# Optimization experiments

Measured on AMD Instinct MI355X. Metric: run time of the kernel, lower is better.

The kernel has to match this reference:

```python
import jax, jax.numpy as jnp
import numpy as np

B, L, D, H = 32, 1024, 1024, 1024

def setup_inputs() -> dict:
    key = jax.random.key(0)
    k1, k2, k3 = jax.random.split(key, 3)
    query = jax.random.normal(k1, (B, L, D), dtype=jnp.float32)
    keys = jax.random.normal(k2, (B, L, D), dtype=jnp.float32)
    # xavier_normal for Linear(D, H): std = sqrt(2/(D+H))
    W = jax.random.normal(k3, (H, D), dtype=jnp.float32) * np.sqrt(2.0 / (D + H)).astype(np.float32)
    b = jnp.zeros((H,), dtype=jnp.float32)
    return {"query": query, "keys": keys, "W": W, "b": b}

def reference(query, keys, W, b):
    # L2-normalize along feature dim (matches torch .norm(dim=-1, keepdim=True))
    qn = query / jnp.linalg.norm(query, axis=-1, keepdims=True)
    kn = keys / jnp.linalg.norm(keys, axis=-1, keepdims=True)
    # scores[b,i,j] = <kn[b,i], qn[b,j]>  ->  [B, Lk, Lq]
    scores = jnp.einsum('bid,bjd->bij', kn, qn)
    attn = jax.nn.softmax(scores, axis=-1)
    # bmm(attn, keys) then sum over batch -> [L, D]
    out = jnp.einsum('bij,bjd->id', attn, keys)
    x = jax.nn.relu(out @ W.T + b)
    return (x, attn)
```

## Files before the change

### kernel.cpp

```cpp
#include <hip/hip_runtime.h>
#include <hip/hip_bf16.h>

#define NBATCH 32
#define Ls 1024
#define Ds 1024
#define Hs 1024

typedef float f32x4 __attribute__((ext_vector_type(4)));
typedef __bf16 v8bf __attribute__((ext_vector_type(8)));
typedef unsigned short u16x8 __attribute__((ext_vector_type(8)));
typedef unsigned short u16x4 __attribute__((ext_vector_type(4)));
typedef __hip_bfloat16 bf16;

__device__ __forceinline__ float bfbits2f(unsigned short h) {
  unsigned u = ((unsigned)h) << 16;
  return __builtin_bit_cast(float, u);
}
__device__ __forceinline__ unsigned short f2b(float x) {
  return __builtin_bit_cast(unsigned short, __float2bfloat16(x));
}
__device__ __forceinline__ u16x8 pack8(const float4& a, const float4& b, float s) {
  u16x8 r;
  r[0] = f2b(a.x * s); r[1] = f2b(a.y * s); r[2] = f2b(a.z * s); r[3] = f2b(a.w * s);
  r[4] = f2b(b.x * s); r[5] = f2b(b.y * s); r[6] = f2b(b.z * s); r[7] = f2b(b.w * s);
  return r;
}

__global__ __launch_bounds__(256) void k_convq(const float* __restrict__ q,
                                               bf16* __restrict__ qn) {
  const int w0 = ((int)blockIdx.x * 256 + (int)threadIdx.x) >> 6;
  const int lane = threadIdx.x & 63;
  #pragma unroll
  for (int it = 0; it < 2; ++it) {
    const size_t r0 = ((size_t)(it * 8192 + w0)) * 2;
    const float4* q0 = reinterpret_cast<const float4*>(q + r0 * Ds);
    float4 qv[2][4];
    #pragma unroll
    for (int rr = 0; rr < 2; ++rr)
      #pragma unroll
      for (int h = 0; h < 2; ++h) {
        qv[rr][h * 2 + 0] = q0[rr * 256 + h * 128 + lane * 2 + 0];
        qv[rr][h * 2 + 1] = q0[rr * 256 + h * 128 + lane * 2 + 1];
      }
    float sq0 = 0.f, sq1 = 0.f;
    #pragma unroll
    for (int p = 0; p < 4; ++p) {
      sq0 += qv[0][p].x*qv[0][p].x + qv[0][p].y*qv[0][p].y + qv[0][p].z*qv[0][p].z + qv[0][p].w*qv[0][p].w;
      sq1 += qv[1][p].x*qv[1][p].x + qv[1][p].y*qv[1][p].y + qv[1][p].z*qv[1][p].z + qv[1][p].w*qv[1][p].w;
    }
    #pragma unroll
    for (int o = 1; o < 64; o <<= 1) { sq0 += __shfl_xor(sq0, o); sq1 += __shfl_xor(sq1, o); }
    const float iq0 = 1.0f / sqrtf(sq0), iq1 = 1.0f / sqrtf(sq1);
    u16x8* qo = reinterpret_cast<u16x8*>(qn + r0 * Ds);
    qo[lane]        = pack8(qv[0][0], qv[0][1], iq0);
    qo[64 + lane]   = pack8(qv[0][2], qv[0][3], iq0);
    qo[128 + lane]  = pack8(qv[1][0], qv[1][1], iq1);
    qo[192 + lane]  = pack8(qv[1][2], qv[1][3], iq1);
  }
}

__global__ __launch_bounds__(256) void k_convkT(const float* __restrict__ k,
                                                bf16* __restrict__ kb,
                                                bf16* __restrict__ kT,
                                                float* __restrict__ invk) {
  __shared__ float tile[64][65];
  __shared__ float red[4][16][16];
  const int b = blockIdx.y;
  const int j0 = blockIdx.x * 64;
  const int t = threadIdx.x;
  const int jr = t >> 4;
  const int cg = t & 15;
  const int c4 = cg * 4;
  const float* src = k + (size_t)b * Ls * Ds + (size_t)j0 * Ds;
  bf16* kbd = kb + (size_t)b * Ls * Ds + (size_t)j0 * Ds;
  bf16* kTd = kT + (size_t)b * Ds * Ls + j0;
  float ssq[4] = {0.f, 0.f, 0.f, 0.f};

  for (int dc = 0; dc < 16; ++dc) {
    const int d0 = dc * 64;
    float4 v[4];
    #pragma unroll
    for (int rr = 0; rr < 4; ++rr) {
      const int j = jr + rr * 16;
      v[rr] = *reinterpret_cast<const float4*>(&src[(size_t)j * Ds + d0 + c4]);
      ssq[rr] += v[rr].x*v[rr].x + v[rr].y*v[rr].y + v[rr].z*v[rr].z + v[rr].w*v[rr].w;
      u16x4 o = { f2b(v[rr].x), f2b(v[rr].y), f2b(v[rr].z), f2b(v[rr].w) };
      *reinterpret_cast<u16x4*>(&kbd[(size_t)j * Ds + d0 + c4]) = o;
    }
    __syncthreads();
    #pragma unroll
    for (int rr = 0; rr < 4; ++rr) {
      const int j = jr + rr * 16;
      tile[j][c4 + 0] = v[rr].x; tile[j][c4 + 1] = v[rr].y;
      tile[j][c4 + 2] = v[rr].z; tile[j][c4 + 3] = v[rr].w;
    }
    __syncthreads();
    #pragma unroll
    for (int rr = 0; rr < 4; ++rr) {
      const int dd = jr + rr * 16;
      u16x4 o = { f2b(tile[c4 + 0][dd]), f2b(tile[c4 + 1][dd]),
                  f2b(tile[c4 + 2][dd]), f2b(tile[c4 + 3][dd]) };
      *reinterpret_cast<u16x4*>(&kTd[(size_t)(d0 + dd) * Ls + c4]) = o;
    }
  }

  #pragma unroll
  for (int rr = 0; rr < 4; ++rr) red[rr][jr][cg] = ssq[rr];
  __syncthreads();
  if (t < 64) {
    const int r = (t & 15) + (t >> 4) * 16;
    float s = 0.f;
    #pragma unroll
    for (int c = 0; c < 16; ++c) s += red[t >> 4][t & 15][c];
    invk[(size_t)b * Ls + j0 + r] = 1.0f / sqrtf(s);
  }
}

__global__ __launch_bounds__(256) void k_w2(const float* __restrict__ W,
                                            bf16* __restrict__ W2) {
  const size_t idx = (size_t)blockIdx.x * 256 + threadIdx.x;
  const size_t e0 = idx * 4;
  const size_t h = e0 >> 10, d = e0 & 1023;
  const float4 w = reinterpret_cast<const float4*>(W)[idx];
  u16x4 wh = { f2b(w.x), f2b(w.y), f2b(w.z), f2b(w.w) };
  u16x4 wl = { f2b(w.x - bfbits2f(wh[0])), f2b(w.y - bfbits2f(wh[1])),
               f2b(w.z - bfbits2f(wh[2])), f2b(w.w - bfbits2f(wh[3])) };
  bf16* row = W2 + h * 3072;
  *reinterpret_cast<u16x4*>(row + d) = wh;
  *reinterpret_cast<u16x4*>(row + 1024 + d) = wh;
  *reinterpret_cast<u16x4*>(row + 2048 + d) = wl;
}

template<int KT, int MODE>
__global__ __launch_bounds__(512) void k_gemm256(
    const bf16* __restrict__ A, const bf16* __restrict__ B,
    void* __restrict__ Cv, const float* __restrict__ scale,
    int lda, int ldb, int ldc, int nb,
    size_t sA, size_t sB, size_t zA, size_t zB, size_t zC, size_t zS)
{
  __shared__ bf16 lds[2][2][256 * 64];
  const int tid = threadIdx.x;
  const int lane = tid & 63;
  const int wid = tid >> 6;
  const int wr = wid >> 2;
  const int wc = wid & 3;
  const size_t m0 = (size_t)blockIdx.y * 256;
  const size_t n0 = (size_t)blockIdx.x * 256;
  const bf16* Az = A + (size_t)blockIdx.z * zA;
  const bf16* Bz = B + (size_t)blockIdx.z * zB;

  const int srow = tid >> 3;
  const int sslot = tid & 7;
  f32x4 acc[8][4] = {};

  auto stageChunk = [&](int tt, int ab, int c, int buf) {
    const int bz = tt / KT;
    const int k0 = (tt - bz * KT) * 64;
    const int row = c * 64 + srow;
    const int ksl = (sslot ^ (row & 7)) * 8;
    const bf16* src = (ab == 0)
        ? (Az + (size_t)bz * sA + (m0 + row) * lda + k0 + ksl)
        : (Bz + (size_t)bz * sB + (n0 + row) * ldb + k0 + ksl);
    __builtin_amdgcn_global_load_lds(
        (const __attribute__((address_space(1))) void*)src,
        (__attribute__((address_space(3))) void*)(&lds[buf][ab][c * 4096 + tid * 8]), 16, 0, 0);
  };

  const int rsel = lane & 15, qd = lane >> 4;
  v8bf a[4][2], b[4][2];

  auto readA = [&](const bf16* As, int mh) {
    #pragma unroll
    for (int m = 0; m < 4; ++m) {
      const int r = wr * 128 + mh * 64 + m * 16 + rsel;
      #pragma unroll
      for (int h = 0; h < 2; ++h) {
        const int s = (h * 4 + qd) ^ (r & 7);
        a[m][h] = *reinterpret_cast<const v8bf*>(reinterpret_cast<const char*>(As) + r * 128 + s * 16);
      }
    }
  };
  auto readB2 = [&](const bf16* Bs, int npair) {
    #pragma unroll
    for (int n = 0; n < 2; ++n) {
      const int r = wc * 64 + (npair * 2 + n) * 16 + rsel;
      #pragma unroll
      for (int h = 0; h < 2; ++h) {
        const int s = (h * 4 + qd) ^ (r & 7);
        b[npair * 2 + n][h] = *reinterpret_cast<const v8bf*>(reinterpret_cast<const char*>(Bs) + r * 128 + s * 16);
      }
    }
  };
  auto mfma8 = [&](int mh, int npair) {
    __builtin_amdgcn_s_setprio(1);
    #pragma unroll
    for (int m = 0; m < 4; ++m)
      #pragma unroll
      for (int n = 0; n < 2; ++n) {
        const int mi = mh * 4 + m, ni = npair * 2 + n;
        acc[mi][ni] = __builtin_amdgcn_mfma_f32_16x16x32_bf16(a[m][0], b[ni][0], acc[mi][ni], 0, 0, 0);
        acc[mi][ni] = __builtin_amdgcn_mfma_f32_16x16x32_bf16(a[m][1], b[ni][1], acc[mi][ni], 0, 0, 0);
      }
    __builtin_amdgcn_s_setprio(0);
  };

  const int T = KT * nb;

  #pragma unroll
  for (int c = 0; c < 4; ++c) stageChunk(0, 0, c, 0);
  #pragma unroll
  for (int c = 0; c < 4; ++c) stageChunk(0, 1, c, 0);
  #pragma unroll
  for (int c = 0; c < 4; ++c) stageChunk(1, 0, c, 1);
  #pragma unroll
  for (int c = 0; c < 4; ++c) stageChunk(1, 1, c, 1);
  asm volatile("s_waitcnt vmcnt(8)" ::: "memory");
  __builtin_amdgcn_s_barrier();

  for (int t = 0; t < T; ++t) {
    const int d = t & 1;
    const bf16* As = lds[d][0];
    const bf16* Bs = lds[d][1];
    const int u = t + 2;
    const bool st = (u < T);

    readA(As, 0); readB2(Bs, 0);
    __builtin_amdgcn_s_barrier(); __builtin_amdgcn_sched_barrier(0);
    mfma8(0, 0);
    __builtin_amdgcn_s_barrier();

    readB2(Bs, 1);
    if (st) { stageChunk(u, 0, 0, d); stageChunk(u, 0, 2, d); }
    __builtin_amdgcn_s_barrier(); __builtin_amdgcn_sched_barrier(0);
    mfma8(0, 1);
    __builtin_amdgcn_s_barrier();

    readA(As, 1);
    if (st) { stageChunk(u, 1, 0, d); stageChunk(u, 1, 1, d); }
    __builtin_amdgcn_s_barrier(); __builtin_amdgcn_sched_barrier(0);
    mfma8(1, 1);
    __builtin_amdgcn_s_barrier();

    if (st) { stageChunk(u, 0, 1, d); stageChunk(u, 0, 3, d);
              stageChunk(u, 1, 2, d); stageChunk(u, 1, 3, d); }
    __builtin_amdgcn_s_barrier(); __builtin_amdgcn_sched_barrier(0);
    mfma8(1, 0);
    if (t < T - 1) {
      if (st) { asm volatile("s_waitcnt vmcnt(8)" ::: "memory"); }
      else    { asm volatile("s_waitcnt vmcnt(0)" ::: "memory"); }
      __builtin_amdgcn_s_barrier();
    }
  }

  if (MODE == 0) {
    float* Cz = (float*)Cv + (size_t)blockIdx.z * zC;
    #pragma unroll
    for (int m = 0; m < 8; ++m) {
      const size_t ri = m0 + wr * 128 + m * 16 + (size_t)((lane >> 4) * 4);
      #pragma unroll
      for (int n = 0; n < 4; ++n) {
        const size_t cj = n0 + wc * 64 + n * 16 + (lane & 15);
        #pragma unroll
        for (int r = 0; r < 4; ++r)
          Cz[(ri + r) * ldc + cj] = acc[m][n][r];
      }
    }
  } else {
    bf16* Cz = (bf16*)Cv + (size_t)blockIdx.z * zC;
    const float* Sz = scale + (size_t)blockIdx.z * zS;
    #pragma unroll
    for (int m = 0; m < 8; ++m) {
      const size_t ri = m0 + wr * 128 + m * 16 + (size_t)((lane >> 4) * 4);
      const float4 ik = *reinterpret_cast<const float4*>(Sz + ri);
      #pragma unroll
      for (int n = 0; n < 4; ++n) {
        const size_t cj = n0 + wc * 64 + n * 16 + (lane & 15);
        Cz[(ri + 0) * ldc + cj] = __float2bfloat16(acc[m][n][0] * ik.x);
        Cz[(ri + 1) * ldc + cj] = __float2bfloat16(acc[m][n][1] * ik.y);
        Cz[(ri + 2) * ldc + cj] = __float2bfloat16(acc[m][n][2] * ik.z);
        Cz[(ri + 3) * ldc + cj] = __float2bfloat16(acc[m][n][3] * ik.w);
      }
    }
  }
}

__global__ __launch_bounds__(256) void k_gemm_nt(
    const bf16* __restrict__ A, const bf16* __restrict__ B,
    float* __restrict__ C,
    int lda, int ldb, int ldc, int K,
    size_t zA, size_t zB, size_t zC)
{
  __shared__ bf16 As[128 * 32];
  __shared__ bf16 Bs[128 * 32];
  const int tid = threadIdx.x;
  const int lane = tid & 63;
  const int wc = (tid >> 6) & 1;
  const int wr = (tid >> 7) & 1;
  const size_t m0 = (size_t)blockIdx.y * 128;
  const size_t n0 = (size_t)blockIdx.x * 128;
  const bf16* Az = A + (size_t)blockIdx.z * zA;
  const bf16* Bz = B + (size_t)blockIdx.z * zB;
  float* Cz = C + (size_t)blockIdx.z * zC;
  f32x4 acc[4][4] = {};

  const int beta0 = tid * 16;
  const int row0 = tid >> 2;
  const int kk0 = ((tid & 3) ^ ((row0 >> 1) & 3)) * 8;
  const int sw = (((lane >> 4) ^ ((lane >> 1) & 3)) << 4);
  const int rsel = lane & 15;

  for (int k0 = 0; k0 < K; k0 += 32) {
    __syncthreads();
    __builtin_amdgcn_global_load_lds(
        (const __attribute__((address_space(1))) void*)(Az + (m0 + row0) * lda + (k0 + kk0)),
        (__attribute__((address_space(3))) void*)(&As[beta0 / 2]), 16, 0, 0);
    __builtin_amdgcn_global_load_lds(
        (const __attribute__((address_space(1))) void*)(Az + (m0 + row0 + 64) * lda + (k0 + kk0)),
        (__attribute__((address_space(3))) void*)(&As[beta0 / 2 + 2048]), 16, 0, 0);
    __builtin_amdgcn_global_load_lds(
        (const __attribute__((address_space(1))) void*)(Bz + (n0 + row0) * ldb + (k0 + kk0)),
        (__attribute__((address_space(3))) void*)(&Bs[beta0 / 2]), 16, 0, 0);
    __builtin_amdgcn_global_load_lds(
        (const __attribute__((address_space(1))) void*)(Bz + (n0 + row0 + 64) * ldb + (k0 + kk0)),
        (__attribute__((address_space(3))) void*)(&Bs[beta0 / 2 + 2048]), 16, 0, 0);
    __syncthreads();

    v8bf af[4], bg[4];
    #pragma unroll
    for (int m = 0; m < 4; ++m) {
      const int rA = wr * 64 + m * 16 + rsel;
      af[m] = *reinterpret_cast<const v8bf*>(reinterpret_cast<const char*>(As) + rA * 64 + sw);
      const int rB = wc * 64 + m * 16 + rsel;
      bg[m] = *reinterpret_cast<const v8bf*>(reinterpret_cast<const char*>(Bs) + rB * 64 + sw);
    }
    #pragma unroll
    for (int m = 0; m < 4; ++m)
      #pragma unroll
      for (int n = 0; n < 4; ++n)
        acc[m][n] = __builtin_amdgcn_mfma_f32_16x16x32_bf16(af[m], bg[n], acc[m][n], 0, 0, 0);
  }

  #pragma unroll
  for (int m = 0; m < 4; ++m) {
    const size_t ri = m0 + wr * 64 + m * 16 + ((lane >> 4) * 4);
    #pragma unroll
    for (int n = 0; n < 4; ++n) {
      const size_t cj = n0 + wc * 64 + n * 16 + (lane & 15);
      #pragma unroll
      for (int r = 0; r < 4; ++r)
        Cz[(ri + r) * ldc + cj] = acc[m][n][r];
    }
  }
}

__global__ __launch_bounds__(256) void k_softmax(const bf16* __restrict__ sc,
                                                 float* __restrict__ attn,
                                                 bf16* __restrict__ abf) {
  const int wave = ((int)blockIdx.x * 256 + (int)threadIdx.x) >> 6;
  const int lane = threadIdx.x & 63;
  for (int i = 0; i < 4; ++i) {
    const size_t row = (size_t)wave * 4 + i;
    const u16x8* sr = reinterpret_cast<const u16x8*>(sc + row * Ls);
    const u16x8 s0 = sr[lane], s1 = sr[lane + 64];
    float e[16];
    float ss = 0.f;
    #pragma unroll
    for (int j = 0; j < 8; ++j) { e[j] = __expf(bfbits2f(s0[j])); ss += e[j]; }
    #pragma unroll
    for (int j = 0; j < 8; ++j) { e[8 + j] = __expf(bfbits2f(s1[j])); ss += e[8 + j]; }
    #pragma unroll
    for (int o = 1; o < 64; o <<= 1) ss += __shfl_xor(ss, o);
    const float inv = 1.0f / ss;
    #pragma unroll
    for (int j = 0; j < 16; ++j) e[j] *= inv;
    float4* ar = reinterpret_cast<float4*>(attn + row * Ls);
    float4 a0 = {e[0], e[1], e[2], e[3]},   a1 = {e[4], e[5], e[6], e[7]};
    float4 a2 = {e[8], e[9], e[10], e[11]}, a3 = {e[12], e[13], e[14], e[15]};
    ar[lane * 2 + 0] = a0;  ar[lane * 2 + 1] = a1;
    ar[128 + lane * 2 + 0] = a2;  ar[128 + lane * 2 + 1] = a3;
    u16x8* ab8 = reinterpret_cast<u16x8*>(abf + row * Ls);
    u16x8 b0, b1;
    #pragma unroll
    for (int j = 0; j < 8; ++j) { b0[j] = f2b(e[j]); b1[j] = f2b(e[8 + j]); }
    ab8[lane] = b0;
    ab8[64 + lane] = b1;
  }
}

__global__ __launch_bounds__(256) void k_reduce(const float* __restrict__ part,
                                                bf16* __restrict__ A2) {
  const size_t idx = (size_t)blockIdx.x * 256 + threadIdx.x;
  float4 s = {0.f, 0.f, 0.f, 0.f};
  #pragma unroll
  for (int g = 0; g < 16; ++g) {
    const float4 p = reinterpret_cast<const float4*>(part + (size_t)g * (Ls * Ds))[idx];
    s.x += p.x; s.y += p.y; s.z += p.z; s.w += p.w;
  }
  const size_t e0 = idx * 4;
  const size_t i = e0 >> 10, d = e0 & 1023;
  u16x4 h = { f2b(s.x), f2b(s.y), f2b(s.z), f2b(s.w) };
  u16x4 l = { f2b(s.x - bfbits2f(h[0])), f2b(s.y - bfbits2f(h[1])),
              f2b(s.z - bfbits2f(h[2])), f2b(s.w - bfbits2f(h[3])) };
  bf16* row = A2 + i * 3072;
  *reinterpret_cast<u16x4*>(row + d) = h;
  *reinterpret_cast<u16x4*>(row + 1024 + d) = l;
  *reinterpret_cast<u16x4*>(row + 2048 + d) = h;
}

__global__ __launch_bounds__(256) void k_reduce2(const float* __restrict__ part2,
                                                 const float* __restrict__ bias,
                                                 float* __restrict__ xout) {
  const size_t idx = (size_t)blockIdx.x * 256 + threadIdx.x;
  float4 s = {0.f, 0.f, 0.f, 0.f};
  #pragma unroll
  for (int g = 0; g < 4; ++g) {
    const float4 p = reinterpret_cast<const float4*>(part2 + (size_t)g * (Ls * Hs))[idx];
    s.x += p.x; s.y += p.y; s.z += p.z; s.w += p.w;
  }
  const size_t h0 = (idx * 4) & 1023;
  const float4 bv = *reinterpret_cast<const float4*>(bias + h0);
  s.x = fmaxf(s.x + bv.x, 0.f); s.y = fmaxf(s.y + bv.y, 0.f);
  s.z = fmaxf(s.z + bv.z, 0.f); s.w = fmaxf(s.w + bv.w, 0.f);
  reinterpret_cast<float4*>(xout)[idx] = s;
}

extern "C" void kernel_launch(void* const* d_in, const int* in_sizes, int n_in,
                              void* d_out, int out_size, void* d_ws, size_t ws_size,
                              hipStream_t stream) {
  const float* q = (const float*)d_in[0];
  const float* k = (const float*)d_in[1];
  const float* W = (const float*)d_in[2];
  const float* bias = (const float*)d_in[3];
  float* xout = (float*)d_out;
  float* attn = (float*)d_out + (size_t)Ls * Hs;

  char* w = (char*)d_ws;
  bf16* qn    = (bf16*)w;
  bf16* kb    = (bf16*)(w + ((size_t)64 << 20));
  bf16* kT    = (bf16*)(w + ((size_t)128 << 20));
  bf16* sc_bf = (bf16*)(w + ((size_t)192 << 20));
  bf16* W2    = (bf16*)(w + ((size_t)256 << 20));
  bf16* A2    = (bf16*)(w + ((size_t)263 << 20));
  float* invk = (float*)(w + ((size_t)270 << 20));
  float* part  = (float*)kb;
  float* part2 = (float*)kT;
  bf16* abf = qn;

  k_convq<<<2048, 256, 0, stream>>>(q, qn);
  k_convkT<<<dim3(16, NBATCH), 256, 0, stream>>>(k, kb, kT, invk);
  k_w2<<<(Hs * Ds / 4) / 256, 256, 0, stream>>>(W, W2);

  k_gemm256<16, 1><<<dim3(4, 4, NBATCH), 512, 0, stream>>>(kb, qn, sc_bf, invk,
      Ds, Ds, Ls, 1,
      (size_t)Ls * Ds, (size_t)Ls * Ds,
      (size_t)Ls * Ds, (size_t)Ls * Ds, (size_t)Ls * Ls, (size_t)Ls);

  k_softmax<<<2048, 256, 0, stream>>>(sc_bf, attn, abf);

  k_gemm256<16, 0><<<dim3(4, 4, 16), 512, 0, stream>>>(abf, kT, part, nullptr,
      Ls, Ls, Ds, 2,
      (size_t)Ls * Ls, (size_t)Ls * Ds,
      (size_t)2 * Ls * Ls, (size_t)2 * Ls * Ds, (size_t)Ls * Ds, 0);

  k_reduce<<<(Ls * Ds / 4) / 256, 256, 0, stream>>>(part, A2);

  k_gemm_nt<<<dim3(8, 8, 4), 256, 0, stream>>>(A2, W2, part2,
      3072, 3072, Hs, 768, 768, 768, (size_t)Ls * Hs);

  k_reduce2<<<(Ls * Hs / 4) / 256, 256, 0, stream>>>(part2, bias, xout);
}
```

Measured before the change: 347.1 us.

## Restructure GEMM main loop to load all LDS fragments upfront with fewer barriers

The inner k-loop now reads both A halves and all B fragments from LDS at the start of each step into separate register sets. MFMA groups are then gated by explicit lgkmcnt waits instead of four barrier-separated phases. All global-to-LDS stage copies are issued together after a single barrier, once the current buffer has been fully read. This is meant to cut barrier count and let LDS reads overlap MFMAs, at the cost of more VGPRs for the extra A fragment set, which could lower occupancy.

```diff
diff --git a/kernel.cpp b/kernel.cpp
--- a/kernel.cpp
+++ b/kernel.cpp
@@ -167,16 +167,16 @@
   };
 
   const int rsel = lane & 15, qd = lane >> 4;
-  v8bf a[4][2], b[4][2];
-
-  auto readA = [&](const bf16* As, int mh) {
+  v8bf a0[4][2], a1[4][2], b[4][2];
+
+  auto readAinto = [&](v8bf (&dst)[4][2], const bf16* As, int mh) {
     #pragma unroll
     for (int m = 0; m < 4; ++m) {
       const int r = wr * 128 + mh * 64 + m * 16 + rsel;
       #pragma unroll
       for (int h = 0; h < 2; ++h) {
         const int s = (h * 4 + qd) ^ (r & 7);
-        a[m][h] = *reinterpret_cast<const v8bf*>(reinterpret_cast<const char*>(As) + r * 128 + s * 16);
+        dst[m][h] = *reinterpret_cast<const v8bf*>(reinterpret_cast<const char*>(As) + r * 128 + s * 16);
       }
     }
   };
@@ -191,15 +191,15 @@
       }
     }
   };
-  auto mfma8 = [&](int mh, int npair) {
+  auto mfmaQ = [&](v8bf (&aa)[4][2], int mh, int npair) {
     __builtin_amdgcn_s_setprio(1);
     #pragma unroll
     for (int m = 0; m < 4; ++m)
       #pragma unroll
       for (int n = 0; n < 2; ++n) {
         const int mi = mh * 4 + m, ni = npair * 2 + n;
-        acc[mi][ni] = __builtin_amdgcn_mfma_f32_16x16x32_bf16(a[m][0], b[ni][0], acc[mi][ni], 0, 0, 0);
-        acc[mi][ni] = __builtin_amdgcn_mfma_f32_16x16x32_bf16(a[m][1], b[ni][1], acc[mi][ni], 0, 0, 0);
+        acc[mi][ni] = __builtin_amdgcn_mfma_f32_16x16x32_bf16(aa[m][0], b[ni][0], acc[mi][ni], 0, 0, 0);
+        acc[mi][ni] = __builtin_amdgcn_mfma_f32_16x16x32_bf16(aa[m][1], b[ni][1], acc[mi][ni], 0, 0, 0);
       }
     __builtin_amdgcn_s_setprio(0);
   };
@@ -224,27 +224,32 @@
     const int u = t + 2;
     const bool st = (u < T);
 
-    readA(As, 0); readB2(Bs, 0);
-    __builtin_amdgcn_s_barrier(); __builtin_amdgcn_sched_barrier(0);
-    mfma8(0, 0);
+    readAinto(a0, As, 0);
+    readB2(Bs, 0);
+    __builtin_amdgcn_sched_barrier(0);
+    readB2(Bs, 1);
+    __builtin_amdgcn_sched_barrier(0);
+    readAinto(a1, As, 1);
+    __builtin_amdgcn_sched_barrier(0);
+
+    asm volatile("s_waitcnt lgkmcnt(12)" ::: "memory");
+    __builtin_amdgcn_sched_barrier(0);
+    mfmaQ(a0, 0, 0);
+    asm volatile("s_waitcnt lgkmcnt(8)" ::: "memory");
+    __builtin_amdgcn_sched_barrier(0);
+    mfmaQ(a0, 0, 1);
+    asm volatile("s_waitcnt lgkmcnt(0)" ::: "memory");
+    __builtin_amdgcn_sched_barrier(0);
     __builtin_amdgcn_s_barrier();
-
-    readB2(Bs, 1);
-    if (st) { stageChunk(u, 0, 0, d); stageChunk(u, 0, 2, d); }
-    __builtin_amdgcn_s_barrier(); __builtin_amdgcn_sched_barrier(0);
-    mfma8(0, 1);
-    __builtin_amdgcn_s_barrier();
-
-    readA(As, 1);
-    if (st) { stageChunk(u, 1, 0, d); stageChunk(u, 1, 1, d); }
-    __builtin_amdgcn_s_barrier(); __builtin_amdgcn_sched_barrier(0);
-    mfma8(1, 1);
-    __builtin_amdgcn_s_barrier();
-
-    if (st) { stageChunk(u, 0, 1, d); stageChunk(u, 0, 3, d);
-              stageChunk(u, 1, 2, d); stageChunk(u, 1, 3, d); }
-    __builtin_amdgcn_s_barrier(); __builtin_amdgcn_sched_barrier(0);
-    mfma8(1, 0);
+    if (st) {
+      stageChunk(u, 0, 0, d); stageChunk(u, 0, 1, d);
+      stageChunk(u, 0, 2, d); stageChunk(u, 0, 3, d);
+      stageChunk(u, 1, 0, d); stageChunk(u, 1, 1, d);
+      stageChunk(u, 1, 2, d); stageChunk(u, 1, 3, d);
+    }
+    __builtin_amdgcn_sched_barrier(0);
+    mfmaQ(a1, 1, 1);
+    mfmaQ(a1, 1, 0);
     if (t < T - 1) {
       if (st) { asm volatile("s_waitcnt vmcnt(8)" ::: "memory"); }
       else    { asm volatile("s_waitcnt vmcnt(0)" ::: "memory"); }
```

After: 349.7 us. Within noise of the previous version (+0.8%).
